# Performance work log

Measured on AMD Instinct MI355X. Metric: run time of the kernel, lower is better.

## Reference

```python
import jax, jax.numpy as jnp
import numpy as np

N_NODES = 100000
N_EDGES = 1600000
D_IN, D_HID, D_OUT = 128, 128, 64


def spmm(row, col, val, h, n):
    # y[i] = sum_{e: row[e]==i} val[e] * h[col[e]]  (A_hat @ h with A in COO form)
    return jax.ops.segment_sum(val[:, None] * h[col], row, num_segments=n)


def setup_inputs() -> dict:
    key = jax.random.key(0)
    ks = jax.random.split(key, 7)
    x = jax.random.normal(ks[0], (1, N_NODES, D_IN), dtype=jnp.float32)
    edge_row = jax.random.randint(ks[1], (N_EDGES,), 0, N_NODES, dtype=jnp.int32)
    edge_col = jax.random.randint(ks[2], (N_EDGES,), 0, N_NODES, dtype=jnp.int32)
    edge_val = jax.random.uniform(ks[3], (N_EDGES,), dtype=jnp.float32)
    W0 = jax.random.normal(ks[4], (D_HID, D_IN), dtype=jnp.float32) * 0.05
    W1 = jax.random.normal(ks[5], (D_HID, D_HID), dtype=jnp.float32) * 0.05
    W2 = jax.random.normal(ks[6], (D_OUT, D_HID), dtype=jnp.float32) * 0.05
    return {"x": x, "edge_row": edge_row, "edge_col": edge_col,
            "edge_val": edge_val, "W0": W0, "W1": W1, "W2": W2}


def reference(x, edge_row, edge_col, edge_val, W0, W1, W2):
    B, N, D = x.shape
    n = B * N
    h = x.reshape(n, D)
    # input conv: Linear (no bias) -> SpMM -> ReLU
    h = jax.nn.relu(spmm(edge_row, edge_col, edge_val, h @ W0.T, n))
    # hidden conv with residual: ReLU(A (h W1^T)) + h
    h = jax.nn.relu(spmm(edge_row, edge_col, edge_val, h @ W1.T, n)) + h
    # dropout is identity in eval mode
    out = spmm(edge_row, edge_col, edge_val, h @ W2.T, n)
    return out
```

## Files before the change

kernel.cpp:

```cpp
#include <hip/hip_runtime.h>


typedef unsigned int u32;
typedef unsigned short u16;
typedef __attribute__((ext_vector_type(8))) short bf16x8;
typedef __attribute__((ext_vector_type(4))) float f32x4;

constexpr int NN = 100000;
constexpr int NE = 1600000;
constexpr int PAD = 100352;
constexpr int NBUCK = 392;
constexpr int BCAP = 4608;
constexpr int EPB = 4096;
constexpr int P1B = (NE + EPB - 1) / EPB;
constexpr int G0B = (NN + 63) / 64;
constexpr int EPT = BCAP / 256;
constexpr int NCB = 13;

__device__ __forceinline__ u16 f2bf(float f) {
    u32 x = __float_as_uint(f);
    x += 0x7fffu + ((x >> 16) & 1u);
    return (u16)(x >> 16);
}

__device__ __forceinline__ void wfrag_one(const float* __restrict__ W,
                                          u16* __restrict__ Wf, int total, int i)
{
    if (i < total) {
        const int j    = i & 7;
        const int lane = (i >> 3) & 63;
        const int kc   = (i >> 9) & 3;
        const int ct   = i >> 11;
        const int src  = (ct * 16 + (lane & 15)) * 128 + kc * 32 + (lane >> 4) * 8 + j;
        Wf[i] = f2bf(W[src]);
    }
}

__global__ __launch_bounds__(256)
void wcvt_kernel(const float* __restrict__ W0, const float* __restrict__ W1,
                 const float* __restrict__ W2, u16* __restrict__ wf0,
                 u16* __restrict__ wf1, u16* __restrict__ wf2,
                 int* __restrict__ bcur)
{
    const int i = blockIdx.x * 256 + threadIdx.x;
    if (i < 512) bcur[i] = 0;
    wfrag_one(W0, wf0, 128 * 128, i);
    wfrag_one(W1, wf1, 128 * 128, i);
    wfrag_one(W2, wf2, 64 * 128, i);
}

__global__ __launch_bounds__(256)
void k1_kernel(const float* __restrict__ x, const u16* __restrict__ Wf,
               u16* __restrict__ Cb,
               const int* __restrict__ erow, const int* __restrict__ ecol,
               const float* __restrict__ eval, int* __restrict__ bcur,
               int2* __restrict__ part)
{
    __shared__ u16 smem[64 * 136];
    const int tid = threadIdx.x;

    if ((int)blockIdx.x < P1B) {
        int* shist = (int*)smem;
        int* sbase = shist + NBUCK;
        for (int i = tid; i < NBUCK; i += 256) shist[i] = 0;
        __syncthreads();

        const int base = blockIdx.x * EPB;
        #pragma unroll
        for (int j = 0; j < EPB / 256; ++j) {
            const int e = base + j * 256 + tid;
            if (e < NE) atomicAdd(&shist[erow[e] >> 8], 1);
        }
        __syncthreads();
        for (int i = tid; i < NBUCK; i += 256) {
            const int c = shist[i];
            sbase[i] = c ? atomicAdd(&bcur[i], c) : 0;
            shist[i] = 0;
        }
        __syncthreads();
        #pragma unroll
        for (int j = 0; j < EPB / 256; ++j) {
            const int e = base + j * 256 + tid;
            if (e < NE) {
                const int r = erow[e];
                const int b = r >> 8;
                const int rk = atomicAdd(&shist[b], 1);
                part[(size_t)b * BCAP + sbase[b] + rk] =
                    make_int2(((r & 255) << 17) | ecol[e], __float_as_int(eval[e]));
            }
        }
        return;
    }

    constexpr int RS   = 136;
    constexpr int PADW = 136;
    u16* sA = smem;
    u16* sC = smem;
    const int w    = tid >> 6;
    const int lane = tid & 63;
    const int m    = lane & 15;
    const int q    = lane >> 4;
    const int rowBase = ((int)blockIdx.x - P1B) * 64;

    #pragma unroll
    for (int i = 0; i < 8; ++i) {
        const int g = (i * 256 + tid) * 4;
        const int r = g >> 7, c = g & 127;
        float4 v = make_float4(0.f, 0.f, 0.f, 0.f);
        if (rowBase + r < NN) v = *(const float4*)(x + (size_t)(rowBase + r) * 128 + c);
        u16* d = &sA[r * RS + c];
        d[0] = f2bf(v.x); d[1] = f2bf(v.y); d[2] = f2bf(v.z); d[3] = f2bf(v.w);
    }
    __syncthreads();

    bf16x8 afrag[4];
    #pragma unroll
    for (int kc = 0; kc < 4; ++kc)
        afrag[kc] = *(const bf16x8*)&sA[(w * 16 + m) * RS + kc * 32 + q * 8];
    __syncthreads();

    #pragma unroll
    for (int ct = 0; ct < 8; ++ct) {
        f32x4 acc = {0.f, 0.f, 0.f, 0.f};
        #pragma unroll
        for (int kc = 0; kc < 4; ++kc) {
            const bf16x8 b = *(const bf16x8*)(Wf + (((ct * 4 + kc) * 64) + lane) * 8);
            acc = __builtin_amdgcn_mfma_f32_16x16x32_bf16(afrag[kc], b, acc, 0, 0, 0);
        }
        #pragma unroll
        for (int r = 0; r < 4; ++r)
            sC[(w * 16 + q * 4 + r) * PADW + ct * 16 + m] = f2bf(acc[r]);
    }
    __syncthreads();

    const int g    = lane >> 2;
    const int cb   = (lane & 3) * 32;
    const int grow = rowBase + w * 16 + g;
    if (grow < NN) {
        #pragma unroll
        for (int i = 0; i < 4; ++i) {
            const int4 v = *(const int4*)&sC[(w * 16 + g) * PADW + cb + i * 8];
            *(int4*)(Cb + (size_t)grow * 128 + cb + i * 8) = v;
        }
    }
}

__global__ __launch_bounds__(256)
void part2_kernel(const int* __restrict__ bcur, const int2* __restrict__ part,
                  int* __restrict__ offs, int2* __restrict__ pce)
{
    __shared__ int scnt[256 * NCB];
    __shared__ int sdata[256];
    __shared__ int2 sout[BCAP];
    const int b = blockIdx.x;
    const int tid = threadIdx.x;

    const int cnt = bcur[b];
    const int2* src = part + (size_t)b * BCAP;

    int2 ed[EPT];
    #pragma unroll
    for (int j = 0; j < EPT; ++j) {
        const int idx = j * 256 + tid;
        ed[j] = (idx < cnt) ? src[idx] : make_int2(-1, 0);
    }

    #pragma unroll
    for (int j = 0; j < NCB; ++j) scnt[j * 256 + tid] = 0;

    int partial = 0;
    for (int i = tid; i < b; i += 256) partial += bcur[i];
    sdata[tid] = partial;
    __syncthreads();
    #pragma unroll
    for (int off = 128; off > 0; off >>= 1) {
        if (tid < off) sdata[tid] += sdata[tid + off];
        __syncthreads();
    }
    const int gb = sdata[0];
    __syncthreads();

    #pragma unroll
    for (int j = 0; j < EPT; ++j) {
        if (ed[j].x >= 0) {
            const int rl = ((u32)ed[j].x) >> 17;
            const int cb = (ed[j].x & 0x1FFFF) >> 13;
            atomicAdd(&scnt[rl * NCB + cb], 1);
        }
    }
    __syncthreads();

    int rsum = 0;
    #pragma unroll
    for (int j = 0; j < NCB; ++j) rsum += scnt[tid * NCB + j];
    sdata[tid] = rsum;
    __syncthreads();
    #pragma unroll
    for (int off = 1; off < 256; off <<= 1) {
        const int val = (tid >= off) ? sdata[tid - off] : 0;
        __syncthreads();
        sdata[tid] += val;
        __syncthreads();
    }
    const int excl = sdata[tid] - rsum;
    offs[b * 256 + tid] = gb + excl;

    int run = excl;
    #pragma unroll
    for (int j = 0; j < NCB; ++j) {
        const int c = scnt[tid * NCB + j];
        scnt[tid * NCB + j] = run;
        run += c;
    }
    __syncthreads();

    #pragma unroll
    for (int j = 0; j < EPT; ++j) {
        if (ed[j].x >= 0) {
            const int rl  = ((u32)ed[j].x) >> 17;
            const int cb  = (ed[j].x & 0x1FFFF) >> 13;
            const int pos = atomicAdd(&scnt[rl * NCB + cb], 1);
            sout[pos] = make_int2(ed[j].x & 0x1FFFF, ed[j].y);
        }
    }
    __syncthreads();

    #pragma unroll
    for (int j = 0; j < EPT; ++j) {
        const int idx = j * 256 + tid;
        if (idx < cnt) pce[(size_t)gb + idx] = sout[idx];
    }
}

template<int LPC>
__device__ __forceinline__ void load_row(const u16* p, u32* u) {
    if constexpr (LPC == 8) {
        const uint4 t = *(const uint4*)p;
        u[0] = t.x; u[1] = t.y; u[2] = t.z; u[3] = t.w;
    } else {
        const uint2 t = *(const uint2*)p;
        u[0] = t.x; u[1] = t.y;
    }
}

template<int LPC>
__device__ __forceinline__ void fma_row(float v, const u32* u, float* a) {
    #pragma unroll
    for (int j = 0; j < LPC / 2; ++j) {
        a[2*j]   = fmaf(v, __uint_as_float(u[j] << 16),         a[2*j]);
        a[2*j+1] = fmaf(v, __uint_as_float(u[j] & 0xffff0000u), a[2*j+1]);
    }
}

template<int DO, int MODE>
__global__ __launch_bounds__(256)
void spmm_gemm(const int* __restrict__ offs, const int2* __restrict__ pce,
               const u16* __restrict__ Hb, const u16* __restrict__ Wf,
               const u16* __restrict__ Res, u16* __restrict__ Cb,
               u16* __restrict__ Hout)
{
    constexpr int RS   = 136;
    constexpr int PADW = DO + 8;
    __shared__ u16 smem[16 * 136];
    const int tid = threadIdx.x;
    const int ln  = tid & 15;
    const int rl  = tid >> 4;
    const int row = blockIdx.x * 16 + rl;

    const int s = offs[row];
    const int t = offs[row + 1];
    const u16* hbase = Hb + ln * 8;

    float a0[8], a1[8];
    #pragma unroll
    for (int j = 0; j < 8; ++j) { a0[j] = 0.f; a1[j] = 0.f; }

    for (int e = s; e < t; e += 16) {
        int2 my = make_int2(0, 0);
        if (e + ln < t) my = pce[e + ln];
        const int rem = t - e;
        #pragma unroll
        for (int qd = 0; qd < 4; ++qd) {
            if (qd * 4 < rem) {
                const int c0 = __shfl(my.x, qd * 4 + 0, 16);
                const int v0 = __shfl(my.y, qd * 4 + 0, 16);
                const int c1 = __shfl(my.x, qd * 4 + 1, 16);
                const int v1 = __shfl(my.y, qd * 4 + 1, 16);
                const int c2 = __shfl(my.x, qd * 4 + 2, 16);
                const int v2 = __shfl(my.y, qd * 4 + 2, 16);
                const int c3 = __shfl(my.x, qd * 4 + 3, 16);
                const int v3 = __shfl(my.y, qd * 4 + 3, 16);
                u32 u0[4], u1[4], u2[4], u3[4];
                load_row<8>(hbase + (size_t)c0 * 128, u0);
                load_row<8>(hbase + (size_t)c1 * 128, u1);
                load_row<8>(hbase + (size_t)c2 * 128, u2);
                load_row<8>(hbase + (size_t)c3 * 128, u3);
                fma_row<8>(__int_as_float(v0), u0, a0);
                fma_row<8>(__int_as_float(v1), u1, a1);
                fma_row<8>(__int_as_float(v2), u2, a0);
                fma_row<8>(__int_as_float(v3), u3, a1);
            }
        }
    }
    #pragma unroll
    for (int j = 0; j < 8; ++j) a0[j] = fmaxf(a0[j] + a1[j], 0.f);

    if constexpr (MODE == 2) {
        u32 r[4];
        load_row<8>(Res + (size_t)row * 128 + ln * 8, r);
        #pragma unroll
        for (int j = 0; j < 4; ++j) {
            a0[2*j]   += __uint_as_float(r[j] << 16);
            a0[2*j+1] += __uint_as_float(r[j] & 0xffff0000u);
        }
    }
    u32 o[4];
    #pragma unroll
    for (int j = 0; j < 4; ++j)
        o[j] = (u32)f2bf(a0[2*j]) | ((u32)f2bf(a0[2*j+1]) << 16);
    const uint4 packed = make_uint4(o[0], o[1], o[2], o[3]);
    *(uint4*)&smem[rl * RS + ln * 8] = packed;
    if constexpr (MODE == 1)
        *(uint4*)(Hout + (size_t)row * 128 + ln * 8) = packed;
    __syncthreads();

    constexpr int TPW = DO / 64;
    const int w    = tid >> 6;
    const int lane = tid & 63;
    const int m    = lane & 15;
    const int q    = lane >> 4;

    bf16x8 afrag[4];
    #pragma unroll
    for (int kc = 0; kc < 4; ++kc)
        afrag[kc] = *(const bf16x8*)&smem[m * RS + kc * 32 + q * 8];

    f32x4 acc[TPW];
    #pragma unroll
    for (int tw = 0; tw < TPW; ++tw) {
        const int ct = w * TPW + tw;
        acc[tw] = (f32x4){0.f, 0.f, 0.f, 0.f};
        #pragma unroll
        for (int kc = 0; kc < 4; ++kc) {
            const bf16x8 b = *(const bf16x8*)(Wf + (((ct * 4 + kc) * 64) + lane) * 8);
            acc[tw] = __builtin_amdgcn_mfma_f32_16x16x32_bf16(afrag[kc], b, acc[tw], 0, 0, 0);
        }
    }
    __syncthreads();

    #pragma unroll
    for (int tw = 0; tw < TPW; ++tw) {
        const int ct = w * TPW + tw;
        #pragma unroll
        for (int r = 0; r < 4; ++r)
            smem[(q * 4 + r) * PADW + ct * 16 + m] = f2bf(acc[tw][r]);
    }
    __syncthreads();

    if (DO == 128 || tid < 128) {
        const int g = tid * 8;
        const int r = g / DO;
        const int c = g % DO;
        const int4 v = *(const int4*)&smem[r * PADW + c];
        *(int4*)(Cb + ((size_t)blockIdx.x * 16 + r) * DO + c) = v;
    }
}

__global__ __launch_bounds__(256)
void spmm_out(const int* __restrict__ offs, const int2* __restrict__ pce,
              const u16* __restrict__ Hb, float* __restrict__ Y)
{
    const int ln  = threadIdx.x & 15;
    const int row = blockIdx.x * 16 + (threadIdx.x >> 4);
    if (row >= NN) return;
    const int s = offs[row];
    const int t = offs[row + 1];
    const u16* hbase = Hb + ln * 4;

    float a0[4], a1[4];
    #pragma unroll
    for (int j = 0; j < 4; ++j) { a0[j] = 0.f; a1[j] = 0.f; }

    for (int e = s; e < t; e += 16) {
        int2 my = make_int2(0, 0);
        if (e + ln < t) my = pce[e + ln];
        const int rem = t - e;
        #pragma unroll
        for (int qd = 0; qd < 4; ++qd) {
            if (qd * 4 < rem) {
                const int c0 = __shfl(my.x, qd * 4 + 0, 16);
                const int v0 = __shfl(my.y, qd * 4 + 0, 16);
                const int c1 = __shfl(my.x, qd * 4 + 1, 16);
                const int v1 = __shfl(my.y, qd * 4 + 1, 16);
                const int c2 = __shfl(my.x, qd * 4 + 2, 16);
                const int v2 = __shfl(my.y, qd * 4 + 2, 16);
                const int c3 = __shfl(my.x, qd * 4 + 3, 16);
                const int v3 = __shfl(my.y, qd * 4 + 3, 16);
                u32 u0[2], u1[2], u2[2], u3[2];
                load_row<4>(hbase + (size_t)c0 * 64, u0);
                load_row<4>(hbase + (size_t)c1 * 64, u1);
                load_row<4>(hbase + (size_t)c2 * 64, u2);
                load_row<4>(hbase + (size_t)c3 * 64, u3);
                fma_row<4>(__int_as_float(v0), u0, a0);
                fma_row<4>(__int_as_float(v1), u1, a1);
                fma_row<4>(__int_as_float(v2), u2, a0);
                fma_row<4>(__int_as_float(v3), u3, a1);
            }
        }
    }
    #pragma unroll
    for (int j = 0; j < 4; ++j) a0[j] += a1[j];
    *(float4*)(Y + (size_t)row * 64 + ln * 4) = make_float4(a0[0], a0[1], a0[2], a0[3]);
}

extern "C" void kernel_launch(void* const* d_in, const int* in_sizes, int n_in,
                              void* d_out, int out_size, void* d_ws, size_t ws_size,
                              hipStream_t stream) {
    const float* x    = (const float*)d_in[0];
    const int*   erow = (const int*)  d_in[1];
    const int*   ecol = (const int*)  d_in[2];
    const float* eval = (const float*)d_in[3];
    const float* W0   = (const float*)d_in[4];
    const float* W1   = (const float*)d_in[5];
    const float* W2   = (const float*)d_in[6];
    float* out = (float*)d_out;

    char* p = (char*)d_ws;
    const size_t BUFB = (size_t)NN * 128 * sizeof(u16);
    u16* t0b  = (u16*)p;  p += BUFB;
    u16* t1b  = (u16*)p;  p += BUFB;
    u16* h1b  = (u16*)p;  p += BUFB;
    u16* wf0  = (u16*)p;  p += 128 * 128 * 2;
    u16* wf1  = (u16*)p;  p += 128 * 128 * 2;
    u16* wf2  = (u16*)p;  p += 64 * 128 * 2;
    int* bcur   = (int*)p; p += 512 * 4;
    int* offs   = (int*)p; p += ((size_t)PAD + 256) * 4;
    int2* part  = (int2*)p; p += (size_t)NBUCK * BCAP * 8;
    int2* pce   = (int2*)p;

    const dim3 blk(256);
    const int rowBlocks = NN / 16;

    wcvt_kernel<<<64, blk, 0, stream>>>(W0, W1, W2, wf0, wf1, wf2, bcur);
    k1_kernel  <<<P1B + G0B, blk, 0, stream>>>(x, wf0, t0b, erow, ecol, eval, bcur, part);
    part2_kernel<<<NBUCK, blk, 0, stream>>>(bcur, part, offs, pce);
    spmm_gemm<128, 1><<<rowBlocks, blk, 0, stream>>>(offs, pce, t0b, wf1, nullptr, t1b, h1b);
    spmm_gemm<64, 2><<<rowBlocks, blk, 0, stream>>>(offs, pce, t1b, wf2, h1b, t0b, nullptr);
    spmm_out<<<rowBlocks, blk, 0, stream>>>(offs, pce, t0b, out);
}
```

Baseline: 315.6 us.

## Partition edges block-locally with per-block bucket offsets instead of global bucket atomics

The first partition pass now writes each block's edges into its own contiguous region, sorted by bucket, and records per-block bucket offsets. This replaces scattered writes into global bucket slots reserved by atomics. The second pass gathers each bucket's runs from every block into shared memory, then scatters the counting-sorted edges straight to their final positions without a staging copy. EPB is doubled so there are fewer partition blocks. The trade-off is a serial per-thread gather of variable-length runs and extra scans, which may load-imbalance part2.

```diff
diff --git a/kernel.cpp b/kernel.cpp
--- a/kernel.cpp
+++ b/kernel.cpp
@@ -11,10 +11,9 @@
 constexpr int PAD = 100352;
 constexpr int NBUCK = 392;
 constexpr int BCAP = 4608;
-constexpr int EPB = 4096;
+constexpr int EPB = 8192;
 constexpr int P1B = (NE + EPB - 1) / EPB;
 constexpr int G0B = (NN + 63) / 64;
-constexpr int EPT = BCAP / 256;
 constexpr int NCB = 13;
 
 __device__ __forceinline__ u16 f2bf(float f) {
@@ -54,38 +53,59 @@
                u16* __restrict__ Cb,
                const int* __restrict__ erow, const int* __restrict__ ecol,
                const float* __restrict__ eval, int* __restrict__ bcur,
-               int2* __restrict__ part)
+               int2* __restrict__ part, int* __restrict__ boffs)
 {
     __shared__ u16 smem[64 * 136];
     const int tid = threadIdx.x;
 
     if ((int)blockIdx.x < P1B) {
         int* shist = (int*)smem;
-        int* sbase = shist + NBUCK;
-        for (int i = tid; i < NBUCK; i += 256) shist[i] = 0;
-        __syncthreads();
-
-        const int base = blockIdx.x * EPB;
+        int* sexcl = shist + 512;
+        int* sdat  = sexcl + 512;
+        const int blk = blockIdx.x;
+        shist[tid] = 0; shist[tid + 256] = 0;
+        __syncthreads();
+
+        const int base = blk * EPB;
         #pragma unroll
         for (int j = 0; j < EPB / 256; ++j) {
             const int e = base + j * 256 + tid;
             if (e < NE) atomicAdd(&shist[erow[e] >> 8], 1);
         }
         __syncthreads();
-        for (int i = tid; i < NBUCK; i += 256) {
-            const int c = shist[i];
-            sbase[i] = c ? atomicAdd(&bcur[i], c) : 0;
-            shist[i] = 0;
-        }
-        __syncthreads();
+
+        const int c0 = shist[2 * tid];
+        const int c1 = shist[2 * tid + 1];
+        if (c0) atomicAdd(&bcur[2 * tid], c0);
+        if (c1) atomicAdd(&bcur[2 * tid + 1], c1);
+        const int tsum = c0 + c1;
+        sdat[tid] = tsum;
+        __syncthreads();
+        #pragma unroll
+        for (int off = 1; off < 256; off <<= 1) {
+            const int v = (tid >= off) ? sdat[tid - off] : 0;
+            __syncthreads();
+            sdat[tid] += v;
+            __syncthreads();
+        }
+        const int excl = sdat[tid] - tsum;
+        sexcl[2 * tid]     = excl;
+        sexcl[2 * tid + 1] = excl + c0;
+        const int total = sdat[255];
+        __syncthreads();
+
+        for (int b = tid; b < NBUCK; b += 256)
+            boffs[(size_t)b * P1B + blk] = sexcl[b];
+        if (tid == 0) boffs[(size_t)NBUCK * P1B + blk] = total;
+
         #pragma unroll
         for (int j = 0; j < EPB / 256; ++j) {
             const int e = base + j * 256 + tid;
             if (e < NE) {
                 const int r = erow[e];
                 const int b = r >> 8;
-                const int rk = atomicAdd(&shist[b], 1);
-                part[(size_t)b * BCAP + sbase[b] + rk] =
+                const int pos = atomicAdd(&sexcl[b], 1);
+                part[(size_t)blk * EPB + pos] =
                     make_int2(((r & 255) << 17) | ecol[e], __float_as_int(eval[e]));
             }
         }
@@ -146,27 +166,15 @@
 }
 
 __global__ __launch_bounds__(256)
-void part2_kernel(const int* __restrict__ bcur, const int2* __restrict__ part,
+void part2_kernel(const int* __restrict__ bcur, const int* __restrict__ boffs,
+                  const int2* __restrict__ part,
                   int* __restrict__ offs, int2* __restrict__ pce)
 {
+    __shared__ int2 sbuf[BCAP];
     __shared__ int scnt[256 * NCB];
     __shared__ int sdata[256];
-    __shared__ int2 sout[BCAP];
     const int b = blockIdx.x;
     const int tid = threadIdx.x;
-
-    const int cnt = bcur[b];
-    const int2* src = part + (size_t)b * BCAP;
-
-    int2 ed[EPT];
-    #pragma unroll
-    for (int j = 0; j < EPT; ++j) {
-        const int idx = j * 256 + tid;
-        ed[j] = (idx < cnt) ? src[idx] : make_int2(-1, 0);
-    }
-
-    #pragma unroll
-    for (int j = 0; j < NCB; ++j) scnt[j * 256 + tid] = 0;
 
     int partial = 0;
     for (int i = tid; i < b; i += 256) partial += bcur[i];
@@ -178,15 +186,37 @@
         __syncthreads();
     }
     const int gb = sdata[0];
-    __syncthreads();
-
-    #pragma unroll
-    for (int j = 0; j < EPT; ++j) {
-        if (ed[j].x >= 0) {
-            const int rl = ((u32)ed[j].x) >> 17;
-            const int cb = (ed[j].x & 0x1FFFF) >> 13;
-            atomicAdd(&scnt[rl * NCB + cb], 1);
-        }
+    const int cnt = bcur[b];
+    __syncthreads();
+
+    int lo = 0, len = 0;
+    if (tid < P1B) {
+        lo  = boffs[(size_t)b * P1B + tid];
+        len = boffs[(size_t)(b + 1) * P1B + tid] - lo;
+    }
+    sdata[tid] = len;
+    __syncthreads();
+    #pragma unroll
+    for (int off = 1; off < 256; off <<= 1) {
+        const int v = (tid >= off) ? sdata[tid - off] : 0;
+        __syncthreads();
+        sdata[tid] += v;
+        __syncthreads();
+    }
+    const int dst = sdata[tid] - len;
+
+    #pragma unroll
+    for (int j = 0; j < NCB; ++j) scnt[j * 256 + tid] = 0;
+
+    if (tid < P1B && len > 0) {
+        const int2* srcp = part + (size_t)tid * EPB + lo;
+        for (int i = 0; i < len; ++i) sbuf[dst + i] = srcp[i];
+    }
+    __syncthreads();
+
+    for (int i = tid; i < cnt; i += 256) {
+        const int xk = sbuf[i].x;
+        atomicAdd(&scnt[(((u32)xk) >> 17) * NCB + ((xk & 0x1FFFF) >> 13)], 1);
     }
     __syncthreads();
 
@@ -197,15 +227,15 @@
     __syncthreads();
     #pragma unroll
     for (int off = 1; off < 256; off <<= 1) {
-        const int val = (tid >= off) ? sdata[tid - off] : 0;
-        __syncthreads();
-        sdata[tid] += val;
+        const int v = (tid >= off) ? sdata[tid - off] : 0;
+        __syncthreads();
+        sdata[tid] += v;
         __syncthreads();
     }
     const int excl = sdata[tid] - rsum;
     offs[b * 256 + tid] = gb + excl;
 
-    int run = excl;
+    int run = gb + excl;
     #pragma unroll
     for (int j = 0; j < NCB; ++j) {
         const int c = scnt[tid * NCB + j];
@@ -214,21 +244,12 @@
     }
     __syncthreads();
 
-    #pragma unroll
-    for (int j = 0; j < EPT; ++j) {
-        if (ed[j].x >= 0) {
-            const int rl  = ((u32)ed[j].x) >> 17;
-            const int cb  = (ed[j].x & 0x1FFFF) >> 13;
-            const int pos = atomicAdd(&scnt[rl * NCB + cb], 1);
-            sout[pos] = make_int2(ed[j].x & 0x1FFFF, ed[j].y);
-        }
-    }
-    __syncthreads();
-
-    #pragma unroll
-    for (int j = 0; j < EPT; ++j) {
-        const int idx = j * 256 + tid;
-        if (idx < cnt) pce[(size_t)gb + idx] = sout[idx];
+    for (int i = tid; i < cnt; i += 256) {
+        const int2 ev = sbuf[i];
+        const int rl = ((u32)ev.x) >> 17;
+        const int cb = (ev.x & 0x1FFFF) >> 13;
+        const int pos = atomicAdd(&scnt[rl * NCB + cb], 1);
+        pce[pos] = make_int2(ev.x & 0x1FFFF, ev.y);
     }
 }
 
@@ -434,16 +455,17 @@
     u16* wf1  = (u16*)p;  p += 128 * 128 * 2;
     u16* wf2  = (u16*)p;  p += 64 * 128 * 2;
     int* bcur   = (int*)p; p += 512 * 4;
+    int* boffs  = (int*)p; p += (size_t)(NBUCK + 1) * P1B * 4;
     int* offs   = (int*)p; p += ((size_t)PAD + 256) * 4;
-    int2* part  = (int2*)p; p += (size_t)NBUCK * BCAP * 8;
+    int2* part  = (int2*)p; p += (size_t)P1B * EPB * 8;
     int2* pce   = (int2*)p;
 
     const dim3 blk(256);
     const int rowBlocks = NN / 16;
 
     wcvt_kernel<<<64, blk, 0, stream>>>(W0, W1, W2, wf0, wf1, wf2, bcur);
-    k1_kernel  <<<P1B + G0B, blk, 0, stream>>>(x, wf0, t0b, erow, ecol, eval, bcur, part);
-    part2_kernel<<<NBUCK, blk, 0, stream>>>(bcur, part, offs, pce);
+    k1_kernel  <<<P1B + G0B, blk, 0, stream>>>(x, wf0, t0b, erow, ecol, eval, bcur, part, boffs);
+    part2_kernel<<<NBUCK, blk, 0, stream>>>(bcur, boffs, part, offs, pce);
     spmm_gemm<128, 1><<<rowBlocks, blk, 0, stream>>>(offs, pce, t0b, wf1, nullptr, t1b, h1b);
     spmm_gemm<64, 2><<<rowBlocks, blk, 0, stream>>>(offs, pce, t1b, wf2, h1b, t0b, nullptr);
     spmm_out<<<rowBlocks, blk, 0, stream>>>(offs, pce, t0b, out);
```

New measurement: 331.0 us. 4.9% more time.
